# Kernel optimization log

Hardware: AMD Instinct MI355X
Metric: run time of the kernel (lower is better)

## Reference

```python
import jax, jax.numpy as jnp
import numpy as np

# Llama-7B-like config with CPSVD split projections
B, S, H = 1, 1024, 4096
NH, HD = 32, 128          # num_heads, head_dim
RANK = 1024               # SVD rank per projection
NCOL = 512                # exactly-kept columns per projection
NSVD = H - NCOL           # SVD-compressed columns
ROPE_BASE = 10000.0
WSCALE = 0.02


def setup_inputs() -> dict:
    key = jax.random.key(0)
    ks = jax.random.split(key, 16)
    hidden_states = jax.random.normal(ks[0], (B, S, H), jnp.float32)
    # causal additive mask (large negative above diagonal)
    causal = jnp.triu(jnp.full((S, S), -1e9, jnp.float32), k=1)
    attention_mask = jnp.broadcast_to(causal, (B, 1, S, S))
    position_ids = jnp.broadcast_to(jnp.arange(S, dtype=jnp.int32), (B, S))
    # disjoint partition of the 4096 input columns: 512 kept, 3584 SVD'd
    col_idx = jnp.arange(0, H, H // NCOL, dtype=jnp.int32)          # [512]
    keep = np.ones(H, dtype=bool); keep[np.asarray(col_idx)] = False
    svd_idx = jnp.asarray(np.nonzero(keep)[0], dtype=jnp.int32)      # [3584]
    # per-projection weights (torch Linear convention: [out, in])
    def w(k, shape):
        return jax.random.normal(k, shape, jnp.float32) * WSCALE
    inp = dict(hidden_states=hidden_states, attention_mask=attention_mask,
               position_ids=position_ids, col_idx=col_idx, svd_idx=svd_idx)
    names = ['q', 'k', 'v', 'o']
    for i, p in enumerate(names):
        inp[f'{p}_v_w'] = w(ks[1 + 3 * i], (RANK, NSVD))   # v_proj: n_svd -> rank
        inp[f'{p}_u_w'] = w(ks[2 + 3 * i], (H, RANK))      # u_proj: rank -> hidden
        inp[f'{p}_col_w'] = w(ks[3 + 3 * i], (H, NCOL))    # col: n_col -> hidden
    return inp


def _split_proj(x, svd_idx, col_idx, v_w, u_w, col_w):
    # x: [B,S,H] -> gather + low-rank (V then U) + exact-column matmul, added
    x_svd = x[..., svd_idx]                                  # [B,S,NSVD]
    x_col = x[..., col_idx]                                  # [B,S,NCOL]
    low = jnp.einsum('bsr,hr->bsh', jnp.einsum('bsn,rn->bsr', x_svd, v_w), u_w)
    return low + jnp.einsum('bsc,hc->bsh', x_col, col_w)     # [B,S,H]


def _rotate_half(x):
    x1, x2 = x[..., : HD // 2], x[..., HD // 2 :]
    return jnp.concatenate((-x2, x1), axis=-1)


def reference(hidden_states, attention_mask, position_ids, col_idx, svd_idx,
              q_v_w, q_u_w, q_col_w, k_v_w, k_u_w, k_col_w,
              v_v_w, v_u_w, v_col_w, o_v_w, o_u_w, o_col_w):
    bsz, q_len, _ = hidden_states.shape

    def heads(t):  # [B,S,H] -> [B,NH,S,HD]
        return t.reshape(bsz, q_len, NH, HD).transpose(0, 2, 1, 3)

    q = heads(_split_proj(hidden_states, svd_idx, col_idx, q_v_w, q_u_w, q_col_w))
    k = heads(_split_proj(hidden_states, svd_idx, col_idx, k_v_w, k_u_w, k_col_w))
    v = heads(_split_proj(hidden_states, svd_idx, col_idx, v_v_w, v_u_w, v_col_w))

    # rotary embedding: direct indexed read of cos/sin tables
    inv_freq = 1.0 / (ROPE_BASE ** (jnp.arange(0, HD, 2, dtype=jnp.float32) / HD))
    ang = jnp.arange(q_len, dtype=jnp.float32)[:, None] * inv_freq[None, :]  # [S,HD/2]
    emb = jnp.concatenate((ang, ang), axis=-1)                               # [S,HD]
    cos = jnp.cos(emb)[position_ids][:, None, :, :]                          # [B,1,S,HD]
    sin = jnp.sin(emb)[position_ids][:, None, :, :]
    q = q * cos + _rotate_half(q) * sin
    k = k * cos + _rotate_half(k) * sin

    scale = 1.0 / jnp.sqrt(jnp.float32(HD))
    attn = jnp.einsum('bhqd,bhkd->bhqk', q, k) * scale
    attn = attn + attention_mask
    attn = jnp.maximum(attn, jnp.finfo(attn.dtype).min)
    attn = jax.nn.softmax(attn.astype(jnp.float32), axis=-1).astype(q.dtype)
    out = jnp.einsum('bhqk,bhkd->bhqd', attn, v)             # [B,NH,S,HD]
    out = out.transpose(0, 2, 1, 3).reshape(bsz, q_len, NH * HD)
    out = _split_proj(out, svd_idx, col_idx, o_v_w, o_u_w, o_col_w)
    return out
```

## Files before the change

kernel.cpp:

```cpp
#include <hip/hip_runtime.h>

typedef __attribute__((ext_vector_type(8))) short short8;
typedef __attribute__((ext_vector_type(4))) float f32x4;
typedef unsigned short u16;
typedef unsigned int u32;
typedef unsigned long long u64;

__device__ __forceinline__ u16 f2bf(float f) {
  u32 u = __builtin_bit_cast(u32, f);
  u32 r = u + 0x7FFFu + ((u >> 16) & 1u);
  return (u16)(r >> 16);
}
__device__ __forceinline__ float bf2f(u16 h) {
  u32 u = ((u32)h) << 16;
  return __builtin_bit_cast(float, u);
}

__device__ __forceinline__ void gload16(const void* g, void* l) {
  __builtin_amdgcn_global_load_lds(
      (const __attribute__((address_space(1))) void*)(u64)g,
      (__attribute__((address_space(3))) void*)(u32)(u64)l,
      16, 0, 0);
}

__global__ void prep_w(const float* __restrict__ qv, const float* __restrict__ qu, const float* __restrict__ qc,
                       const float* __restrict__ kv, const float* __restrict__ ku, const float* __restrict__ kc,
                       const float* __restrict__ vv, const float* __restrict__ vu, const float* __restrict__ vc,
                       const float* __restrict__ ov, const float* __restrict__ ou, const float* __restrict__ oc,
                       u16* __restrict__ W1q, u16* __restrict__ W1o,
                       u16* __restrict__ W2q, u16* __restrict__ W2o) {
  long i = (long)blockIdx.x * 256 + threadIdx.x;
  if (i < 3670016L) {
    int which = (int)(i / 917504);
    int j = (int)(i % 917504);
    const float* src = which == 0 ? qv : which == 1 ? kv : which == 2 ? vv : ov;
    u16* dst = which < 3 ? W1q + (long)which * 3670016 : W1o;
    float4 v = ((const float4*)src)[j];
    ushort4 o;
    o.x = f2bf(v.x); o.y = f2bf(v.y); o.z = f2bf(v.z); o.w = f2bf(v.w);
    ((ushort4*)dst)[j] = o;
  } else {
    long j2 = i - 3670016L;
    int which = (int)(j2 / 1572864);
    int rem = (int)(j2 % 1572864);
    int r = rem / 384, c4 = rem % 384;
    const float* u = which == 0 ? qu : which == 1 ? ku : which == 2 ? vu : ou;
    const float* cc = which == 0 ? qc : which == 1 ? kc : which == 2 ? vc : oc;
    u16* dst = which < 3 ? W2q + (long)which * 6291456 : W2o;
    float4 v = (c4 < 256) ? ((const float4*)(u + (long)r * 1024))[c4]
                          : ((const float4*)(cc + (long)r * 512))[c4 - 256];
    ushort4 o;
    o.x = f2bf(v.x); o.y = f2bf(v.y); o.z = f2bf(v.z); o.w = f2bf(v.w);
    ((ushort4*)(dst + (long)r * 1536))[c4] = o;
  }
}

__global__ void gather_in(const float* __restrict__ hid, const int* __restrict__ svd,
                          const int* __restrict__ col, u16* __restrict__ Xs,
                          u16* __restrict__ X2) {
  int s = blockIdx.x;
  const float* row = hid + (long)s * 4096;
  for (int j = threadIdx.x; j < 3584; j += blockDim.x)
    Xs[(long)s * 3584 + j] = f2bf(row[svd[j]]);
  for (int c = threadIdx.x; c < 512; c += blockDim.x) {
    u16 v = f2bf(row[col[c]]);
    X2[(long)s * 1536 + 1024 + c] = v;
    X2[1024L * 1536 + (long)s * 1536 + 1024 + c] = v;
    X2[2 * 1024L * 1536 + (long)s * 1536 + 1024 + c] = v;
  }
}

__global__ void rope2(const u16* __restrict__ P, u16* __restrict__ Qh, u16* __restrict__ Kh) {
  int t = blockIdx.x * 256 + threadIdx.x;
  int which = t >> 21;
  int rem = t & 2097151;
  int d0 = rem & 63, s = (rem >> 6) & 1023, h = rem >> 16;
  const u16* src = P + (long)which * 4194304;
  float x1 = bf2f(src[(long)s * 4096 + h * 128 + d0]);
  float x2 = bf2f(src[(long)s * 4096 + h * 128 + d0 + 64]);
  float inv = exp2f(-(float)d0 * 0.20762050593046013f);
  float ang = (float)s * inv;
  float sn = __sinf(ang), cs = __cosf(ang);
  float scale = which ? 1.0f : (0.08838834764831845f * 1.44269504088896340f);
  u16* dst = which ? Kh : Qh;
  long o = ((long)h * 1024 + s) * 128 + d0;
  dst[o] = f2bf((x1 * cs - x2 * sn) * scale);
  dst[o + 64] = f2bf((x2 * cs + x1 * sn) * scale);
}

__global__ void vtrans(const u16* __restrict__ P, u16* __restrict__ Vt) {
  __shared__ u16 t[64][65];
  int h = blockIdx.z, d0 = blockIdx.y * 64, s0 = blockIdx.x * 64;
  int c = threadIdx.x & 63, r0 = threadIdx.x >> 6;
  for (int r = r0; r < 64; r += 4)
    t[r][c] = P[(long)(s0 + r) * 4096 + h * 128 + d0 + c];
  __syncthreads();
  for (int r = r0; r < 64; r += 4)
    Vt[(long)(h * 128 + d0 + r) * 1024 + s0 + c] = t[c][r];
}

template <int FOUT>
__global__ __launch_bounds__(256) void gemm_nt(const u16* __restrict__ A,
                                               const u16* __restrict__ B,
                                               void* __restrict__ Cv, int K, int ldc,
                                               long sAz, long sBz, long sCz) {
  __shared__ __align__(16) u16 As[128 * 64];
  __shared__ __align__(16) u16 Bs[128 * 64];
  const int tid = threadIdx.x;
  const int w = tid >> 6, lane = tid & 63;
  const int wr = w >> 1, wc = w & 1;
  const int lr = lane & 15, lk = lane >> 4;
  const u16* Ab = A + (long)blockIdx.z * sAz + (long)blockIdx.y * 128 * K;
  const u16* Bb = B + (long)blockIdx.z * sBz + (long)blockIdx.x * 128 * K;
  const int srow = w * 8 + (lane >> 3);
  const int scol = (lane & 7) * 8;

  f32x4 acc[4][4] = {};

  for (int k0 = 0; k0 < K; k0 += 64) {
#pragma unroll
    for (int i = 0; i < 4; ++i) {
      gload16(Ab + (long)(i * 32 + srow) * K + k0 + scol, &As[i * 2048 + w * 512]);
      gload16(Bb + (long)(i * 32 + srow) * K + k0 + scol, &Bs[i * 2048 + w * 512]);
    }
    __syncthreads();
#pragma unroll
    for (int kk = 0; kk < 2; ++kk) {
      short8 af[4], bf[4];
#pragma unroll
      for (int m = 0; m < 4; ++m)
        af[m] = *(const short8*)&As[(wr * 64 + m * 16 + lr) * 64 + kk * 32 + lk * 8];
#pragma unroll
      for (int n = 0; n < 4; ++n)
        bf[n] = *(const short8*)&Bs[(wc * 64 + n * 16 + lr) * 64 + kk * 32 + lk * 8];
#pragma unroll
      for (int m = 0; m < 4; ++m)
#pragma unroll
        for (int n = 0; n < 4; ++n)
          acc[m][n] = __builtin_amdgcn_mfma_f32_16x16x32_bf16(af[m], bf[n], acc[m][n], 0, 0, 0);
    }
    __syncthreads();
  }

  const long crow = (long)blockIdx.y * 128 + wr * 64 + lk * 4;
  const long ccol = (long)blockIdx.x * 128 + wc * 64 + lr;
  if constexpr (FOUT == 0) {
    u16* C = (u16*)Cv + (long)blockIdx.z * sCz;
#pragma unroll
    for (int m = 0; m < 4; ++m)
#pragma unroll
      for (int n = 0; n < 4; ++n)
#pragma unroll
        for (int j = 0; j < 4; ++j)
          C[(crow + m * 16 + j) * ldc + ccol + n * 16] = f2bf(acc[m][n][j]);
  } else {
    float* C = (float*)Cv + (long)blockIdx.z * sCz;
#pragma unroll
    for (int m = 0; m < 4; ++m)
#pragma unroll
      for (int n = 0; n < 4; ++n)
#pragma unroll
        for (int j = 0; j < 4; ++j)
          C[(crow + m * 16 + j) * ldc + ccol + n * 16] = acc[m][n][j];
  }
}

__global__ __launch_bounds__(256) void attn_k(const u16* __restrict__ Qh,
                                              const u16* __restrict__ Kh,
                                              const u16* __restrict__ Vt,
                                              float* __restrict__ Op,
                                              float* __restrict__ Lp) {
  const int p = blockIdx.x, h = blockIdx.z;
  const int w = threadIdx.x >> 6, lane = threadIdx.x & 63;
  const int r = w & 1, c = blockIdx.y * 2 + (w >> 1);
  const int lr = lane & 15, lk = lane >> 4;
  __shared__ __align__(16) u16 Plds[4][16][72];

#pragma unroll
  for (int ph = 0; ph < 2; ++ph) {
    const int qt = ph ? 31 - p : p;
    const int q0 = qt * 32 + r * 16;
    const int ktmax = q0 >> 6;
    short8 qf[4];
#pragma unroll
    for (int kk = 0; kk < 4; ++kk)
      qf[kk] = *(const short8*)&Qh[((long)h * 1024 + q0 + lr) * 128 + kk * 32 + lk * 8];
    f32x4 oacc[8] = {};
    float lsum[4] = {0.f, 0.f, 0.f, 0.f};
    for (int kt = c; kt <= ktmax; kt += 4) {
      const int k0 = kt * 64;
      f32x4 sacc[4] = {};
#pragma unroll
      for (int ct = 0; ct < 4; ++ct) {
        const u16* kp = &Kh[((long)h * 1024 + k0 + ct * 16 + lr) * 128 + lk * 8];
#pragma unroll
        for (int kk = 0; kk < 4; ++kk) {
          short8 kf = *(const short8*)&kp[kk * 32];
          sacc[ct] = __builtin_amdgcn_mfma_f32_16x16x32_bf16(qf[kk], kf, sacc[ct], 0, 0, 0);
        }
      }
      if (kt == ktmax) {
#pragma unroll
        for (int ct = 0; ct < 4; ++ct)
#pragma unroll
          for (int j = 0; j < 4; ++j)
            if (k0 + ct * 16 + lr > q0 + lk * 4 + j) sacc[ct][j] = -3.0e38f;
      }
#pragma unroll
      for (int ct = 0; ct < 4; ++ct)
#pragma unroll
        for (int j = 0; j < 4; ++j) {
          float pv = exp2f(sacc[ct][j]);
          sacc[ct][j] = pv;
          lsum[j] += pv;
        }
#pragma unroll
      for (int ct = 0; ct < 4; ++ct)
#pragma unroll
        for (int j = 0; j < 4; ++j)
          Plds[w][lk * 4 + j][ct * 16 + lr] = f2bf(sacc[ct][j]);
      short8 pf0 = *(const short8*)&Plds[w][lr][lk * 8];
      short8 pf1 = *(const short8*)&Plds[w][lr][32 + lk * 8];
#pragma unroll
      for (int dt = 0; dt < 8; ++dt) {
        const u16* vp = &Vt[((long)h * 128 + dt * 16 + lr) * 1024 + k0 + lk * 8];
        short8 vf0 = *(const short8*)&vp[0];
        oacc[dt] = __builtin_amdgcn_mfma_f32_16x16x32_bf16(pf0, vf0, oacc[dt], 0, 0, 0);
        short8 vf1 = *(const short8*)&vp[32];
        oacc[dt] = __builtin_amdgcn_mfma_f32_16x16x32_bf16(pf1, vf1, oacc[dt], 0, 0, 0);
      }
    }
#pragma unroll
    for (int j = 0; j < 4; ++j) {
      float v = lsum[j];
      v += __shfl_xor(v, 1); v += __shfl_xor(v, 2);
      v += __shfl_xor(v, 4); v += __shfl_xor(v, 8);
      int q = q0 + lk * 4 + j;
      long ob = ((long)c * 32 + h) * 1024 + q;
      if (lr == 0) Lp[ob] = v;
#pragma unroll
      for (int dt = 0; dt < 8; ++dt)
        Op[ob * 128 + dt * 16 + lr] = oacc[dt][j];
    }
  }
}

__global__ void merge_k(const float* __restrict__ Op, const float* __restrict__ Lp,
                        u16* __restrict__ Xso, u16* __restrict__ X2o) {
  int t = blockIdx.x * 256 + threadIdx.x;
  int d4 = t & 31, s = (t >> 5) & 1023, h = t >> 15;
  long base = ((long)h * 1024 + s) * 32 + d4;
  float4 a = {0.f, 0.f, 0.f, 0.f};
  float l = 0.f;
#pragma unroll
  for (int c = 0; c < 4; ++c) {
    float4 v = ((const float4*)Op)[(long)c * 1048576 + base];
    a.x += v.x; a.y += v.y; a.z += v.z; a.w += v.w;
    l += Lp[((long)c * 32 + h) * 1024 + s];
  }
  float inv = 1.f / l;
  int H0 = h * 128 + d4 * 4;
  float av[4] = {a.x, a.y, a.z, a.w};
#pragma unroll
  for (int e = 0; e < 4; ++e) {
    int H = H0 + e;
    u16 b = f2bf(av[e] * inv);
    if ((H & 7) == 0) X2o[(long)s * 1536 + 1024 + (H >> 3)] = b;
    else Xso[(long)s * 3584 + H - (H >> 3) - 1] = b;
  }
}

extern "C" void kernel_launch(void* const* d_in, const int* in_sizes, int n_in,
                              void* d_out, int out_size, void* d_ws, size_t ws_size,
                              hipStream_t stream) {
  (void)in_sizes; (void)n_in; (void)out_size; (void)ws_size;
  const float* hid = (const float*)d_in[0];
  const int* colI = (const int*)d_in[3];
  const int* svdI = (const int*)d_in[4];
  const float* W[12];
  for (int i = 0; i < 12; ++i) W[i] = (const float*)d_in[5 + i];

  char* ws = (char*)d_ws;
  u16* W1q = (u16*)(ws + 0);
  u16* W2q = (u16*)(ws + 22020096);
  u16* P   = (u16*)(ws + 59768832);
  float* Op = (float*)(ws + 0);
  float* Lp = (float*)(ws + 67108864);
  u16* W1o = (u16*)(ws + 84934656);
  u16* W2o = (u16*)(ws + 92274688);
  u16* Xs  = (u16*)(ws + 104857600);
  u16* X2  = (u16*)(ws + 112197632);
  u16* Qh  = (u16*)(ws + 124780544);
  u16* Kh  = (u16*)(ws + 133169152);
  u16* Vt  = (u16*)(ws + 141557760);
  u16* Xso = (u16*)(ws + 149946368);

  prep_w<<<38912, 256, 0, stream>>>(W[0], W[1], W[2], W[3], W[4], W[5],
                                    W[6], W[7], W[8], W[9], W[10], W[11],
                                    W1q, W1o, W2q, W2o);
  gather_in<<<1024, 256, 0, stream>>>(hid, svdI, colI, Xs, X2);

  gemm_nt<0><<<dim3(8, 8, 3), 256, 0, stream>>>(Xs, W1q, X2, 3584, 1536, 0L,
                                                1024L * 3584, 1024L * 1536);
  gemm_nt<0><<<dim3(32, 8, 3), 256, 0, stream>>>(X2, W2q, P, 1536, 4096,
                                                 1024L * 1536, 4096L * 1536, 1024L * 4096);
  rope2<<<16384, 256, 0, stream>>>(P, Qh, Kh);
  vtrans<<<dim3(16, 2, 32), 256, 0, stream>>>(P + 2UL * 1024 * 4096, Vt);

  attn_k<<<dim3(16, 2, 32), 256, 0, stream>>>(Qh, Kh, Vt, Op, Lp);
  merge_k<<<4096, 256, 0, stream>>>(Op, Lp, Xso, X2 + 3UL * 1024 * 1536);

  gemm_nt<0><<<dim3(8, 8, 1), 256, 0, stream>>>(Xso, W1o, X2 + 3UL * 1024 * 1536, 3584,
                                                1536, 0L, 0L, 0L);
  gemm_nt<1><<<dim3(32, 8, 1), 256, 0, stream>>>(X2 + 3UL * 1024 * 1536, W2o, d_out,
                                                 1536, 4096, 0L, 0L, 0L);
}
```

Baseline: 605.3 us.

## Fuse attention merge into attention kernel and add BM=64 GEMM tiles

Attention no longer splits the key range four ways with partial outputs and a separate merge kernel. Each wave now walks its full causal key range, normalises in-register and writes bf16 directly into the o-projection gather layout. The QK product is transposed so P stays in registers via packed bf16 converts, removing the LDS round-trip, and blocks are mapped so heads spread across XCDs. Skinny GEMMs gain a BM=64 tile variant for more blocks. The costs are less key parallelism per query, which may leave long causal rows imbalanced, and smaller-tile GEMMs that reuse data less.

```diff
diff --git a/kernel.cpp b/kernel.cpp
--- a/kernel.cpp
+++ b/kernel.cpp
@@ -14,6 +14,11 @@
 __device__ __forceinline__ float bf2f(u16 h) {
   u32 u = ((u32)h) << 16;
   return __builtin_bit_cast(float, u);
+}
+__device__ __forceinline__ u32 cvtpk(float lo, float hi) {
+  u32 r;
+  asm("v_cvt_pk_bf16_f32 %0, %1, %2" : "=v"(r) : "v"(lo), "v"(hi));
+  return r;
 }
 
 __device__ __forceinline__ void gload16(const void* g, void* l) {
@@ -99,42 +104,44 @@
     Vt[(long)(h * 128 + d0 + r) * 1024 + s0 + c] = t[c][r];
 }
 
-template <int FOUT>
+template <int BM, int FOUT>
 __global__ __launch_bounds__(256) void gemm_nt(const u16* __restrict__ A,
                                                const u16* __restrict__ B,
                                                void* __restrict__ Cv, int K, int ldc,
                                                long sAz, long sBz, long sCz) {
-  __shared__ __align__(16) u16 As[128 * 64];
+  __shared__ __align__(16) u16 As[BM * 64];
   __shared__ __align__(16) u16 Bs[128 * 64];
+  constexpr int MF = BM / 32;
   const int tid = threadIdx.x;
   const int w = tid >> 6, lane = tid & 63;
   const int wr = w >> 1, wc = w & 1;
   const int lr = lane & 15, lk = lane >> 4;
-  const u16* Ab = A + (long)blockIdx.z * sAz + (long)blockIdx.y * 128 * K;
+  const u16* Ab = A + (long)blockIdx.z * sAz + (long)blockIdx.y * BM * K;
   const u16* Bb = B + (long)blockIdx.z * sBz + (long)blockIdx.x * 128 * K;
   const int srow = w * 8 + (lane >> 3);
   const int scol = (lane & 7) * 8;
 
-  f32x4 acc[4][4] = {};
+  f32x4 acc[MF][4] = {};
 
   for (int k0 = 0; k0 < K; k0 += 64) {
 #pragma unroll
-    for (int i = 0; i < 4; ++i) {
+    for (int i = 0; i < BM / 32; ++i)
       gload16(Ab + (long)(i * 32 + srow) * K + k0 + scol, &As[i * 2048 + w * 512]);
+#pragma unroll
+    for (int i = 0; i < 4; ++i)
       gload16(Bb + (long)(i * 32 + srow) * K + k0 + scol, &Bs[i * 2048 + w * 512]);
-    }
     __syncthreads();
 #pragma unroll
     for (int kk = 0; kk < 2; ++kk) {
-      short8 af[4], bf[4];
-#pragma unroll
-      for (int m = 0; m < 4; ++m)
-        af[m] = *(const short8*)&As[(wr * 64 + m * 16 + lr) * 64 + kk * 32 + lk * 8];
+      short8 af[MF], bf[4];
+#pragma unroll
+      for (int m = 0; m < MF; ++m)
+        af[m] = *(const short8*)&As[(wr * (BM / 2) + m * 16 + lr) * 64 + kk * 32 + lk * 8];
 #pragma unroll
       for (int n = 0; n < 4; ++n)
         bf[n] = *(const short8*)&Bs[(wc * 64 + n * 16 + lr) * 64 + kk * 32 + lk * 8];
 #pragma unroll
-      for (int m = 0; m < 4; ++m)
+      for (int m = 0; m < MF; ++m)
 #pragma unroll
         for (int n = 0; n < 4; ++n)
           acc[m][n] = __builtin_amdgcn_mfma_f32_16x16x32_bf16(af[m], bf[n], acc[m][n], 0, 0, 0);
@@ -142,12 +149,12 @@
     __syncthreads();
   }
 
-  const long crow = (long)blockIdx.y * 128 + wr * 64 + lk * 4;
+  const long crow = (long)blockIdx.y * BM + wr * (BM / 2) + lk * 4;
   const long ccol = (long)blockIdx.x * 128 + wc * 64 + lr;
   if constexpr (FOUT == 0) {
     u16* C = (u16*)Cv + (long)blockIdx.z * sCz;
 #pragma unroll
-    for (int m = 0; m < 4; ++m)
+    for (int m = 0; m < MF; ++m)
 #pragma unroll
       for (int n = 0; n < 4; ++n)
 #pragma unroll
@@ -156,7 +163,7 @@
   } else {
     float* C = (float*)Cv + (long)blockIdx.z * sCz;
 #pragma unroll
-    for (int m = 0; m < 4; ++m)
+    for (int m = 0; m < MF; ++m)
 #pragma unroll
       for (int n = 0; n < 4; ++n)
 #pragma unroll
@@ -168,35 +175,44 @@
 __global__ __launch_bounds__(256) void attn_k(const u16* __restrict__ Qh,
                                               const u16* __restrict__ Kh,
                                               const u16* __restrict__ Vt,
-                                              float* __restrict__ Op,
-                                              float* __restrict__ Lp) {
-  const int p = blockIdx.x, h = blockIdx.z;
+                                              u16* __restrict__ Xso,
+                                              u16* __restrict__ X2o) {
+  const int bid = blockIdx.x;
+  const int xcd = bid & 7, t = bid >> 3;
+  const int p = t & 15, hg = t >> 4;
+  const int h = hg * 8 + xcd;
   const int w = threadIdx.x >> 6, lane = threadIdx.x & 63;
-  const int r = w & 1, c = blockIdx.y * 2 + (w >> 1);
   const int lr = lane & 15, lk = lane >> 4;
-  __shared__ __align__(16) u16 Plds[4][16][72];
+  const int rh = w >> 1;
 
 #pragma unroll
   for (int ph = 0; ph < 2; ++ph) {
-    const int qt = ph ? 31 - p : p;
-    const int q0 = qt * 32 + r * 16;
+    const int qt = ((w & 1) ^ ph) ? p : 31 - p;
+    const int q0 = qt * 32 + rh * 16;
     const int ktmax = q0 >> 6;
+    const u16* qp = &Qh[((long)h * 1024 + q0 + lr) * 128 + lk * 8];
     short8 qf[4];
 #pragma unroll
-    for (int kk = 0; kk < 4; ++kk)
-      qf[kk] = *(const short8*)&Qh[((long)h * 1024 + q0 + lr) * 128 + kk * 32 + lk * 8];
+    for (int kk = 0; kk < 4; ++kk) qf[kk] = *(const short8*)&qp[kk * 32];
     f32x4 oacc[8] = {};
-    float lsum[4] = {0.f, 0.f, 0.f, 0.f};
-    for (int kt = c; kt <= ktmax; kt += 4) {
+    float lsum = 0.f;
+
+    for (int kt = 0; kt <= ktmax; ++kt) {
       const int k0 = kt * 64;
-      f32x4 sacc[4] = {};
+      f32x4 sacc[4];
 #pragma unroll
       for (int ct = 0; ct < 4; ++ct) {
-        const u16* kp = &Kh[((long)h * 1024 + k0 + ct * 16 + lr) * 128 + lk * 8];
-#pragma unroll
-        for (int kk = 0; kk < 4; ++kk) {
-          short8 kf = *(const short8*)&kp[kk * 32];
-          sacc[ct] = __builtin_amdgcn_mfma_f32_16x16x32_bf16(qf[kk], kf, sacc[ct], 0, 0, 0);
+        if (k0 + ct * 16 > q0 + 15) {
+          sacc[ct] = f32x4{-3.0e38f, -3.0e38f, -3.0e38f, -3.0e38f};
+        } else {
+          f32x4 s = {};
+          const u16* kp = &Kh[((long)h * 1024 + k0 + ct * 16 + lr) * 128 + lk * 8];
+#pragma unroll
+          for (int kk = 0; kk < 4; ++kk) {
+            short8 kf = *(const short8*)&kp[kk * 32];
+            s = __builtin_amdgcn_mfma_f32_16x16x32_bf16(kf, qf[kk], s, 0, 0, 0);
+          }
+          sacc[ct] = s;
         }
       }
       if (kt == ktmax) {
@@ -204,7 +220,7 @@
         for (int ct = 0; ct < 4; ++ct)
 #pragma unroll
           for (int j = 0; j < 4; ++j)
-            if (k0 + ct * 16 + lr > q0 + lk * 4 + j) sacc[ct][j] = -3.0e38f;
+            if (k0 + ct * 16 + lk * 4 + j > q0 + lr) sacc[ct][j] = -3.0e38f;
       }
 #pragma unroll
       for (int ct = 0; ct < 4; ++ct)
@@ -212,61 +228,45 @@
         for (int j = 0; j < 4; ++j) {
           float pv = exp2f(sacc[ct][j]);
           sacc[ct][j] = pv;
-          lsum[j] += pv;
+          lsum += pv;
         }
-#pragma unroll
-      for (int ct = 0; ct < 4; ++ct)
-#pragma unroll
-        for (int j = 0; j < 4; ++j)
-          Plds[w][lk * 4 + j][ct * 16 + lr] = f2bf(sacc[ct][j]);
-      short8 pf0 = *(const short8*)&Plds[w][lr][lk * 8];
-      short8 pf1 = *(const short8*)&Plds[w][lr][32 + lk * 8];
+      union U8 { short8 s; u32 u[4]; };
+      U8 pf0, pf1;
+      pf0.u[0] = cvtpk(sacc[0][0], sacc[0][1]); pf0.u[1] = cvtpk(sacc[0][2], sacc[0][3]);
+      pf0.u[2] = cvtpk(sacc[1][0], sacc[1][1]); pf0.u[3] = cvtpk(sacc[1][2], sacc[1][3]);
+      pf1.u[0] = cvtpk(sacc[2][0], sacc[2][1]); pf1.u[1] = cvtpk(sacc[2][2], sacc[2][3]);
+      pf1.u[2] = cvtpk(sacc[3][0], sacc[3][1]); pf1.u[3] = cvtpk(sacc[3][2], sacc[3][3]);
 #pragma unroll
       for (int dt = 0; dt < 8; ++dt) {
-        const u16* vp = &Vt[((long)h * 128 + dt * 16 + lr) * 1024 + k0 + lk * 8];
-        short8 vf0 = *(const short8*)&vp[0];
-        oacc[dt] = __builtin_amdgcn_mfma_f32_16x16x32_bf16(pf0, vf0, oacc[dt], 0, 0, 0);
-        short8 vf1 = *(const short8*)&vp[32];
-        oacc[dt] = __builtin_amdgcn_mfma_f32_16x16x32_bf16(pf1, vf1, oacc[dt], 0, 0, 0);
+        const u16* vp = &Vt[((long)h * 128 + dt * 16 + lr) * 1024 + k0 + lk * 4];
+        union U8 vf0, vf1;
+        uint2 a0 = *(const uint2*)(vp);
+        uint2 a1 = *(const uint2*)(vp + 16);
+        uint2 b0 = *(const uint2*)(vp + 32);
+        uint2 b1 = *(const uint2*)(vp + 48);
+        vf0.u[0] = a0.x; vf0.u[1] = a0.y; vf0.u[2] = a1.x; vf0.u[3] = a1.y;
+        vf1.u[0] = b0.x; vf1.u[1] = b0.y; vf1.u[2] = b1.x; vf1.u[3] = b1.y;
+        oacc[dt] = __builtin_amdgcn_mfma_f32_16x16x32_bf16(pf0.s, vf0.s, oacc[dt], 0, 0, 0);
+        oacc[dt] = __builtin_amdgcn_mfma_f32_16x16x32_bf16(pf1.s, vf1.s, oacc[dt], 0, 0, 0);
       }
     }
+
+    lsum += __shfl_xor(lsum, 16);
+    lsum += __shfl_xor(lsum, 32);
+    float linv[4];
+#pragma unroll
+    for (int j = 0; j < 4; ++j) linv[j] = 1.f / __shfl(lsum, lk * 4 + j);
 #pragma unroll
     for (int j = 0; j < 4; ++j) {
-      float v = lsum[j];
-      v += __shfl_xor(v, 1); v += __shfl_xor(v, 2);
-      v += __shfl_xor(v, 4); v += __shfl_xor(v, 8);
-      int q = q0 + lk * 4 + j;
-      long ob = ((long)c * 32 + h) * 1024 + q;
-      if (lr == 0) Lp[ob] = v;
-#pragma unroll
-      for (int dt = 0; dt < 8; ++dt)
-        Op[ob * 128 + dt * 16 + lr] = oacc[dt][j];
+      const int q = q0 + lk * 4 + j;
+#pragma unroll
+      for (int dt = 0; dt < 8; ++dt) {
+        const int H = h * 128 + dt * 16 + lr;
+        u16 b = f2bf(oacc[dt][j] * linv[j]);
+        if ((H & 7) == 0) X2o[(long)q * 1536 + 1024 + (H >> 3)] = b;
+        else Xso[(long)q * 3584 + H - (H >> 3) - 1] = b;
+      }
     }
-  }
-}
-
-__global__ void merge_k(const float* __restrict__ Op, const float* __restrict__ Lp,
-                        u16* __restrict__ Xso, u16* __restrict__ X2o) {
-  int t = blockIdx.x * 256 + threadIdx.x;
-  int d4 = t & 31, s = (t >> 5) & 1023, h = t >> 15;
-  long base = ((long)h * 1024 + s) * 32 + d4;
-  float4 a = {0.f, 0.f, 0.f, 0.f};
-  float l = 0.f;
-#pragma unroll
-  for (int c = 0; c < 4; ++c) {
-    float4 v = ((const float4*)Op)[(long)c * 1048576 + base];
-    a.x += v.x; a.y += v.y; a.z += v.z; a.w += v.w;
-    l += Lp[((long)c * 32 + h) * 1024 + s];
-  }
-  float inv = 1.f / l;
-  int H0 = h * 128 + d4 * 4;
-  float av[4] = {a.x, a.y, a.z, a.w};
-#pragma unroll
-  for (int e = 0; e < 4; ++e) {
-    int H = H0 + e;
-    u16 b = f2bf(av[e] * inv);
-    if ((H & 7) == 0) X2o[(long)s * 1536 + 1024 + (H >> 3)] = b;
-    else Xso[(long)s * 3584 + H - (H >> 3) - 1] = b;
   }
 }
 
@@ -284,8 +284,6 @@
   u16* W1q = (u16*)(ws + 0);
   u16* W2q = (u16*)(ws + 22020096);
   u16* P   = (u16*)(ws + 59768832);
-  float* Op = (float*)(ws + 0);
-  float* Lp = (float*)(ws + 67108864);
   u16* W1o = (u16*)(ws + 84934656);
   u16* W2o = (u16*)(ws + 92274688);
   u16* Xs  = (u16*)(ws + 104857600);
@@ -294,24 +292,22 @@
   u16* Kh  = (u16*)(ws + 133169152);
   u16* Vt  = (u16*)(ws + 141557760);
   u16* Xso = (u16*)(ws + 149946368);
+  u16* X2o = X2 + 3UL * 1024 * 1536;
 
   prep_w<<<38912, 256, 0, stream>>>(W[0], W[1], W[2], W[3], W[4], W[5],
                                     W[6], W[7], W[8], W[9], W[10], W[11],
                                     W1q, W1o, W2q, W2o);
   gather_in<<<1024, 256, 0, stream>>>(hid, svdI, colI, Xs, X2);
 
-  gemm_nt<0><<<dim3(8, 8, 3), 256, 0, stream>>>(Xs, W1q, X2, 3584, 1536, 0L,
-                                                1024L * 3584, 1024L * 1536);
-  gemm_nt<0><<<dim3(32, 8, 3), 256, 0, stream>>>(X2, W2q, P, 1536, 4096,
-                                                 1024L * 1536, 4096L * 1536, 1024L * 4096);
+  gemm_nt<64, 0><<<dim3(8, 16, 3), 256, 0, stream>>>(Xs, W1q, X2, 3584, 1536, 0L,
+                                                     1024L * 3584, 1024L * 1536);
+  gemm_nt<128, 0><<<dim3(32, 8, 3), 256, 0, stream>>>(X2, W2q, P, 1536, 4096,
+                                                      1024L * 1536, 4096L * 1536, 1024L * 4096);
   rope2<<<16384, 256, 0, stream>>>(P, Qh, Kh);
   vtrans<<<dim3(16, 2, 32), 256, 0, stream>>>(P + 2UL * 1024 * 4096, Vt);
 
-  attn_k<<<dim3(16, 2, 32), 256, 0, stream>>>(Qh, Kh, Vt, Op, Lp);
-  merge_k<<<4096, 256, 0, stream>>>(Op, Lp, Xso, X2 + 3UL * 1024 * 1536);
-
-  gemm_nt<0><<<dim3(8, 8, 1), 256, 0, stream>>>(Xso, W1o, X2 + 3UL * 1024 * 1536, 3584,
-                                                1536, 0L, 0L, 0L);
-  gemm_nt<1><<<dim3(32, 8, 1), 256, 0, stream>>>(X2 + 3UL * 1024 * 1536, W2o, d_out,
-                                                 1536, 4096, 0L, 0L, 0L);
-}
+  attn_k<<<512, 256, 0, stream>>>(Qh, Kh, Vt, Xso, X2o);
+
+  gemm_nt<64, 0><<<dim3(8, 16, 1), 256, 0, stream>>>(Xso, W1o, X2o, 3584, 1536, 0L, 0L, 0L);
+  gemm_nt<64, 1><<<dim3(32, 16, 1), 256, 0, stream>>>(X2o, W2o, d_out, 1536, 4096, 0L, 0L, 0L);
+}
```

After: 637.2 us. 5.3% more time.
